# Optimization experiments

Measured on AMD Instinct MI355X. Metric: run time of the kernel, lower is better.

The kernel has to match this reference:

```python
import jax, jax.numpy as jnp
import numpy as np

IN_FEATURES = 64
OUT_FEATURES = 64

def setup_inputs() -> dict:
    key = jax.random.key(0)
    kx, kw = jax.random.split(key)
    x = jax.random.normal(kx, (32, 32, 32, IN_FEATURES), dtype=jnp.float32)
    # quadratic weight: [out_features, in_features * in_features]
    W = jax.random.normal(kw, (OUT_FEATURES, IN_FEATURES * IN_FEATURES), dtype=jnp.float32) * 0.02
    return {"x": x, "W": W}

def reference(x, W):
    # Original: outer = x[..., :, None] * x[..., None, :] -> [B,D1,D2,F*F]; then linear(W).
    # Equivalent fused bilinear contraction: out_o = sum_{f,g} x_f x_g W_{o,f,g}
    F_ = x.shape[-1]
    Wr = W.reshape(W.shape[0], F_, F_)  # [O, F, F]
    return jnp.einsum('bacf,bacg,ofg->baco', x, x, Wr)
```

## Files before the change

### kernel.cpp

```cpp
#include <hip/hip_runtime.h>

typedef __attribute__((ext_vector_type(8))) short bf16x8;
typedef __attribute__((ext_vector_type(4))) float f32x4;

constexpr int KPK = 2304;
constexpr int QK  = 576;
constexpr int NCH = 18;

__device__ __forceinline__ unsigned short bf_rne(float f) {
  unsigned u = __float_as_uint(f);
  return (unsigned short)((u + 0x7fffu + ((u >> 16) & 1u)) >> 16);
}

__global__ __launch_bounds__(256) void wprep_kernel(const float* __restrict__ W,
                                                    unsigned short* __restrict__ Wp) {
  int e = blockIdx.x * 256 + threadIdx.x;
  int o = e / KPK;
  int k = e - o * KPK;
  int kq = k / QK;
  int r = k - kq * QK;
  int j = r >> 6, i = r & 63;
  int run1 = 8 - kq;
  int G, F;
  if (j < run1) { G = 7 - kq; F = j; } else { G = kq; F = j - run1; }
  int f = F * 8 + (i >> 3), g = G * 8 + (i & 7);
  float v = W[o * 4096 + f * 64 + g];
  if (F != G) v += W[o * 4096 + g * 64 + f];
  Wp[o * KPK + k] = bf_rne(v);
}

__global__ __launch_bounds__(256, 2) void quad_kernel(const float* __restrict__ x,
                                                      const unsigned short* __restrict__ Wp,
                                                      float* __restrict__ out) {
  __shared__ alignas(16) char smem[65536];
  float* xT = reinterpret_cast<float*>(smem);

  const int t = threadIdx.x;
  const int lane = t & 63;
  const int kq = t >> 6;
  const int q = lane >> 4;
  const int r16 = lane & 15;
  const int pxbase = blockIdx.x * 64;

  char* ring = smem + 16384 + kq * 12288;

  const char* wsrc = reinterpret_cast<const char*>(Wp) +
                     (lane >> 2) * (KPK * 2) + (lane & 3) * 16 + kq * (QK * 2);

  auto issue = [&](int c, int slot) {
    const char* s = wsrc + c * 64;
    char* d = ring + slot * 4096;
#pragma unroll
    for (int i = 0; i < 4; ++i) {
      __builtin_amdgcn_global_load_lds(
          (const __attribute__((address_space(1))) void*)(s + i * (16 * KPK * 2)),
          (__attribute__((address_space(3))) void*)(d + i * 1024), 16, 0, 0);
    }
  };

  issue(0, 0);
  issue(1, 1);

  {
    const float* xg_ = x + (long)pxbase * 64;
#pragma unroll
    for (int c = 0; c < 4; ++c) {
      int e = c * 256 + t;
      int px = e >> 4;
      int f0 = (e & 15) * 4;
      float4 v = *reinterpret_cast<const float4*>(xg_ + px * 64 + f0);
      xT[(f0 + 0) * 64 + (px ^ (f0 + 0))] = v.x;
      xT[(f0 + 1) * 64 + (px ^ (f0 + 1))] = v.y;
      xT[(f0 + 2) * 64 + (px ^ (f0 + 2))] = v.z;
      xT[(f0 + 3) * 64 + (px ^ (f0 + 3))] = v.w;
    }
  }
  __syncthreads();

  float xg[4][8];
  auto load_xg = [&](int G) {
#pragma unroll
    for (int m = 0; m < 4; ++m) {
      int px = m * 16 + r16;
#pragma unroll
      for (int b = 0; b < 8; ++b) {
        int row = G * 8 + b;
        xg[m][b] = xT[row * 64 + (px ^ row)];
      }
    }
  };
  const int run1 = 8 - kq;
  load_xg(7 - kq);

  f32x4 acc[4][4] = {};
  int slot = 0;

  for (int j = 0; j < NCH; ++j) {
    int islot = slot + 2 - ((slot >= 1) ? 3 : 0);
    if (j + 2 < NCH) issue(j + 2, islot);

    if (j < NCH - 2)       asm volatile("s_waitcnt vmcnt(8)" ::: "memory");
    else if (j == NCH - 2) asm volatile("s_waitcnt vmcnt(4)" ::: "memory");
    else                   asm volatile("s_waitcnt vmcnt(0)" ::: "memory");

    const int s = j & 1;
    const int blk = j >> 1;
    const int F = (blk < run1) ? blk : blk - run1;
    if (j == 2 * run1) load_xg(kq);

    const char* wb = ring + slot * 4096;
    bf16x8 bfr[4];
#pragma unroll
    for (int nt = 0; nt < 4; ++nt)
      bfr[nt] = *reinterpret_cast<const bf16x8*>(wb + (nt * 16 + r16) * 64 + q * 16);

    const int row = F * 8 + s * 4 + q;
    bf16x8 afr[4];
#pragma unroll
    for (int m = 0; m < 4; ++m) {
      float xf = xT[row * 64 + ((m * 16 + r16) ^ row)];
      union { unsigned u[4]; bf16x8 v; } pk;
#pragma unroll
      for (int i = 0; i < 4; ++i) {
        unsigned p0 = __float_as_uint(xf * xg[m][2 * i]);
        unsigned p1 = __float_as_uint(xf * xg[m][2 * i + 1]);
        pk.u[i] = __builtin_amdgcn_perm(p1, p0, 0x07060302u);
      }
      afr[m] = pk.v;
    }

#pragma unroll
    for (int nt = 0; nt < 4; ++nt)
#pragma unroll
      for (int m = 0; m < 4; ++m)
        acc[m][nt] = __builtin_amdgcn_mfma_f32_16x16x32_bf16(afr[m], bfr[nt], acc[m][nt], 0, 0, 0);

    slot = (slot == 2) ? 0 : slot + 1;
  }

  __syncthreads();
  float* red = reinterpret_cast<float*>(smem);
#pragma unroll
  for (int m = 0; m < 4; ++m)
#pragma unroll
    for (int nt = 0; nt < 4; ++nt)
      *reinterpret_cast<f32x4*>(red + (m * 4 + kq) * 1024 + (nt * 16 + r16) * 16 + q * 4) =
          acc[m][nt];
  __syncthreads();
  {
    const float* base = red + kq * 4096;
#pragma unroll
    for (int nt = 0; nt < 4; ++nt) {
      int off = (nt * 16 + r16) * 16 + q * 4;
      f32x4 ssum = *reinterpret_cast<const f32x4*>(base + off);
#pragma unroll
      for (int w = 1; w < 4; ++w)
        ssum += *reinterpret_cast<const f32x4*>(base + w * 1024 + off);
      long prow = pxbase + kq * 16 + q * 4;
#pragma unroll
      for (int b = 0; b < 4; ++b)
        out[(prow + b) * 64 + nt * 16 + r16] = ssum[b];
    }
  }
}

extern "C" void kernel_launch(void* const* d_in, const int* in_sizes, int n_in,
                              void* d_out, int out_size, void* d_ws, size_t ws_size,
                              hipStream_t stream) {
  const float* x = (const float*)d_in[0];
  const float* W = (const float*)d_in[1];
  float* out = (float*)d_out;
  unsigned short* Wp = (unsigned short*)d_ws;

  hipLaunchKernelGGL(wprep_kernel, dim3(576), dim3(256), 0, stream, W, Wp);
  hipLaunchKernelGGL(quad_kernel, dim3(512), dim3(256), 0, stream, x, Wp, out);
}
```

Measured before the change: 26.34 us.

## Pre-swizzle weights into MFMA fragment order and load B directly to registers

The weight prep kernel now writes the packed bf16 weights in the exact per-lane MFMA fragment order, so the main kernel can fetch B operands straight into registers with coalesced 16-byte loads. This replaces the LDS ring filled by global_load_lds and its manual vmcnt waits with a three-deep register prefetch. Blocks double to 512 threads covering 128 pixels, so each weight chunk is reused by two wave groups. The reduction is split into two passes to fit the smaller shared buffer. The cost is higher register pressure from the buffered B fragments and from the larger block.

```diff
diff --git a/kernel.cpp b/kernel.cpp
--- a/kernel.cpp
+++ b/kernel.cpp
@@ -15,64 +15,66 @@
 __global__ __launch_bounds__(256) void wprep_kernel(const float* __restrict__ W,
                                                     unsigned short* __restrict__ Wp) {
   int e = blockIdx.x * 256 + threadIdx.x;
-  int o = e / KPK;
-  int k = e - o * KPK;
-  int kq = k / QK;
-  int r = k - kq * QK;
-  int j = r >> 6, i = r & 63;
+  int c = e & 2047;
+  int t2 = e >> 11;
+  int kq = t2 / 18;
+  int j = t2 - kq * 18;
+  int nt = c >> 9;
+  int q = (c >> 7) & 3;
+  int r16 = (c >> 3) & 15;
+  int el = c & 7;
+  int o = nt * 16 + r16;
+  int kl = j * 32 + q * 8 + el;
+  int jblk = kl >> 6, i = kl & 63;
   int run1 = 8 - kq;
   int G, F;
-  if (j < run1) { G = 7 - kq; F = j; } else { G = kq; F = j - run1; }
+  if (jblk < run1) { G = 7 - kq; F = jblk; } else { G = kq; F = jblk - run1; }
   int f = F * 8 + (i >> 3), g = G * 8 + (i & 7);
   float v = W[o * 4096 + f * 64 + g];
   if (F != G) v += W[o * 4096 + g * 64 + f];
-  Wp[o * KPK + k] = bf_rne(v);
+  Wp[e] = bf_rne(v);
 }
 
-__global__ __launch_bounds__(256, 2) void quad_kernel(const float* __restrict__ x,
+__global__ __launch_bounds__(512, 2) void quad_kernel(const float* __restrict__ x,
                                                       const unsigned short* __restrict__ Wp,
                                                       float* __restrict__ out) {
-  __shared__ alignas(16) char smem[65536];
-  float* xT = reinterpret_cast<float*>(smem);
+  __shared__ float xT[8192];
+  __shared__ alignas(16) float red[16384];
 
   const int t = threadIdx.x;
   const int lane = t & 63;
-  const int kq = t >> 6;
+  const int wv = t >> 6;
+  const int kq = wv & 3;
+  const int ph = wv >> 2;
   const int q = lane >> 4;
   const int r16 = lane & 15;
-  const int pxbase = blockIdx.x * 64;
+  const int pxbase = blockIdx.x * 128;
 
-  char* ring = smem + 16384 + kq * 12288;
+  const char* wsrc = reinterpret_cast<const char*>(Wp) + kq * (NCH * 4096) + lane * 16;
 
-  const char* wsrc = reinterpret_cast<const char*>(Wp) +
-                     (lane >> 2) * (KPK * 2) + (lane & 3) * 16 + kq * (QK * 2);
-
-  auto issue = [&](int c, int slot) {
-    const char* s = wsrc + c * 64;
-    char* d = ring + slot * 4096;
+  auto loadB = [&](int j, bf16x8 (&b)[4]) {
 #pragma unroll
-    for (int i = 0; i < 4; ++i) {
-      __builtin_amdgcn_global_load_lds(
-          (const __attribute__((address_space(1))) void*)(s + i * (16 * KPK * 2)),
-          (__attribute__((address_space(3))) void*)(d + i * 1024), 16, 0, 0);
-    }
+    for (int nt = 0; nt < 4; ++nt)
+      b[nt] = *reinterpret_cast<const bf16x8*>(wsrc + j * 4096 + nt * 1024);
   };
 
-  issue(0, 0);
-  issue(1, 1);
+  bf16x8 bufs[3][4];
+  loadB(0, bufs[0]);
+  loadB(1, bufs[1]);
+  loadB(2, bufs[2]);
 
   {
     const float* xg_ = x + (long)pxbase * 64;
 #pragma unroll
     for (int c = 0; c < 4; ++c) {
-      int e = c * 256 + t;
-      int px = e >> 4;
-      int f0 = (e & 15) * 4;
-      float4 v = *reinterpret_cast<const float4*>(xg_ + px * 64 + f0);
-      xT[(f0 + 0) * 64 + (px ^ (f0 + 0))] = v.x;
-      xT[(f0 + 1) * 64 + (px ^ (f0 + 1))] = v.y;
-      xT[(f0 + 2) * 64 + (px ^ (f0 + 2))] = v.z;
-      xT[(f0 + 3) * 64 + (px ^ (f0 + 3))] = v.w;
+      int e4 = c * 512 + t;
+      int px = e4 >> 4;
+      int f0 = (e4 & 15) * 4;
+      float4 v = *reinterpret_cast<const float4*>(xg_ + e4 * 4);
+      xT[(f0 + 0) * 128 + (px ^ (f0 + 0))] = v.x;
+      xT[(f0 + 1) * 128 + (px ^ (f0 + 1))] = v.y;
+      xT[(f0 + 2) * 128 + (px ^ (f0 + 2))] = v.z;
+      xT[(f0 + 3) * 128 + (px ^ (f0 + 3))] = v.w;
     }
   }
   __syncthreads();
@@ -81,11 +83,11 @@
   auto load_xg = [&](int G) {
 #pragma unroll
     for (int m = 0; m < 4; ++m) {
-      int px = m * 16 + r16;
+      int px = ph * 64 + m * 16 + r16;
 #pragma unroll
       for (int b = 0; b < 8; ++b) {
         int row = G * 8 + b;
-        xg[m][b] = xT[row * 64 + (px ^ row)];
+        xg[m][b] = xT[row * 128 + (px ^ row)];
       }
     }
   };
@@ -93,73 +95,65 @@
   load_xg(7 - kq);
 
   f32x4 acc[4][4] = {};
-  int slot = 0;
-
-  for (int j = 0; j < NCH; ++j) {
-    int islot = slot + 2 - ((slot >= 1) ? 3 : 0);
-    if (j + 2 < NCH) issue(j + 2, islot);
-
-    if (j < NCH - 2)       asm volatile("s_waitcnt vmcnt(8)" ::: "memory");
-    else if (j == NCH - 2) asm volatile("s_waitcnt vmcnt(4)" ::: "memory");
-    else                   asm volatile("s_waitcnt vmcnt(0)" ::: "memory");
-
-    const int s = j & 1;
-    const int blk = j >> 1;
-    const int F = (blk < run1) ? blk : blk - run1;
-    if (j == 2 * run1) load_xg(kq);
-
-    const char* wb = ring + slot * 4096;
-    bf16x8 bfr[4];
-#pragma unroll
-    for (int nt = 0; nt < 4; ++nt)
-      bfr[nt] = *reinterpret_cast<const bf16x8*>(wb + (nt * 16 + r16) * 64 + q * 16);
-
-    const int row = F * 8 + s * 4 + q;
-    bf16x8 afr[4];
-#pragma unroll
-    for (int m = 0; m < 4; ++m) {
-      float xf = xT[row * 64 + ((m * 16 + r16) ^ row)];
-      union { unsigned u[4]; bf16x8 v; } pk;
-#pragma unroll
-      for (int i = 0; i < 4; ++i) {
-        unsigned p0 = __float_as_uint(xf * xg[m][2 * i]);
-        unsigned p1 = __float_as_uint(xf * xg[m][2 * i + 1]);
-        pk.u[i] = __builtin_amdgcn_perm(p1, p0, 0x07060302u);
-      }
-      afr[m] = pk.v;
-    }
 
 #pragma unroll
-    for (int nt = 0; nt < 4; ++nt)
+  for (int j = 0; j < NCH; ++j) {
+    if (j == 2 * run1) load_xg(kq);
+    {
+      const int s = j & 1;
+      const int blk = j >> 1;
+      const int F = (blk < run1) ? blk : blk - run1;
+      const int row = F * 8 + s * 4 + q;
+      bf16x8 afr[4];
 #pragma unroll
-      for (int m = 0; m < 4; ++m)
-        acc[m][nt] = __builtin_amdgcn_mfma_f32_16x16x32_bf16(afr[m], bfr[nt], acc[m][nt], 0, 0, 0);
-
-    slot = (slot == 2) ? 0 : slot + 1;
+      for (int m = 0; m < 4; ++m) {
+        float xf = xT[row * 128 + ((ph * 64 + m * 16 + r16) ^ row)];
+        union { unsigned u[4]; bf16x8 v; } pk;
+#pragma unroll
+        for (int i = 0; i < 4; ++i) {
+          unsigned p0 = __float_as_uint(xf * xg[m][2 * i]);
+          unsigned p1 = __float_as_uint(xf * xg[m][2 * i + 1]);
+          pk.u[i] = __builtin_amdgcn_perm(p1, p0, 0x07060302u);
+        }
+        afr[m] = pk.v;
+      }
+#pragma unroll
+      for (int nt = 0; nt < 4; ++nt)
+#pragma unroll
+        for (int m = 0; m < 4; ++m)
+          acc[m][nt] = __builtin_amdgcn_mfma_f32_16x16x32_bf16(afr[m], bufs[j % 3][nt],
+                                                               acc[m][nt], 0, 0, 0);
+    }
+    if (j + 3 < NCH) loadB(j + 3, bufs[j % 3]);
   }
 
-  __syncthreads();
-  float* red = reinterpret_cast<float*>(smem);
 #pragma unroll
-  for (int m = 0; m < 4; ++m)
+  for (int r = 0; r < 2; ++r) {
+    if (r) __syncthreads();
 #pragma unroll
-    for (int nt = 0; nt < 4; ++nt)
-      *reinterpret_cast<f32x4*>(red + (m * 4 + kq) * 1024 + (nt * 16 + r16) * 16 + q * 4) =
-          acc[m][nt];
-  __syncthreads();
-  {
-    const float* base = red + kq * 4096;
+    for (int mm = 0; mm < 2; ++mm)
 #pragma unroll
-    for (int nt = 0; nt < 4; ++nt) {
-      int off = (nt * 16 + r16) * 16 + q * 4;
-      f32x4 ssum = *reinterpret_cast<const f32x4*>(base + off);
+      for (int nt = 0; nt < 4; ++nt)
+        *reinterpret_cast<f32x4*>(red + ((ph * 2 + mm) * 4 + kq) * 1024 +
+                                  (nt * 16 + r16) * 16 + q * 4) = acc[2 * r + mm][nt];
+    __syncthreads();
+    {
+      const int mm2 = kq >> 1;
+      const int h = kq & 1;
+      const float* base = red + (ph * 2 + mm2) * 4 * 1024;
 #pragma unroll
-      for (int w = 1; w < 4; ++w)
-        ssum += *reinterpret_cast<const f32x4*>(base + w * 1024 + off);
-      long prow = pxbase + kq * 16 + q * 4;
+      for (int nh = 0; nh < 2; ++nh) {
+        int nt = h * 2 + nh;
+        int off = (nt * 16 + r16) * 16 + q * 4;
+        f32x4 ssum = *reinterpret_cast<const f32x4*>(base + off);
 #pragma unroll
-      for (int b = 0; b < 4; ++b)
-        out[(prow + b) * 64 + nt * 16 + r16] = ssum[b];
+        for (int w = 1; w < 4; ++w)
+          ssum += *reinterpret_cast<const f32x4*>(base + w * 1024 + off);
+        long prow = pxbase + ph * 64 + (2 * r + mm2) * 16 + q * 4;
+#pragma unroll
+        for (int b = 0; b < 4; ++b)
+          out[(prow + b) * 64 + nt * 16 + r16] = ssum[b];
+      }
     }
   }
 }
@@ -173,5 +167,5 @@
   unsigned short* Wp = (unsigned short*)d_ws;
 
   hipLaunchKernelGGL(wprep_kernel, dim3(576), dim3(256), 0, stream, W, Wp);
-  hipLaunchKernelGGL(quad_kernel, dim3(512), dim3(256), 0, stream, x, Wp, out);
+  hipLaunchKernelGGL(quad_kernel, dim3(256), dim3(512), 0, stream, x, Wp, out);
 }
```

Result: faster. 24.09 us (-8.5%).
